# Performance work log

Hardware: AMD Instinct MI355X
Metric: run time of the kernel (lower is better)

Reference implementation:

```python
import jax, jax.numpy as jnp
import numpy as np

NEG_SLOPE = 0.2  # PyG GATConv default leaky_relu slope


def _gat_conv(x, src, dst, W, a_src, a_dst, b, num_nodes):
    # Linear transform: [N, F_out]
    h = x @ W
    # Per-node attention halves (heads=1): [N]
    alpha_s = h @ a_src
    alpha_d = h @ a_dst
    # Per-edge raw score for edge j->i: a_src.h_j + a_dst.h_i
    e = jax.nn.leaky_relu(alpha_s[src] + alpha_d[dst], NEG_SLOPE)
    # Softmax over edges grouped by destination node (numerically stable)
    m = jax.ops.segment_max(e, dst, num_segments=num_nodes)
    ex = jnp.exp(e - m[dst])
    denom = jax.ops.segment_sum(ex, dst, num_segments=num_nodes)
    coef = ex / denom[dst]
    # Attention-weighted aggregation of source features into destinations
    out = jax.ops.segment_sum(h[src] * coef[:, None], dst, num_segments=num_nodes)
    return out + b


def setup_inputs() -> dict:
    key = jax.random.key(0)
    ks = jax.random.split(key, 12)
    N, F_in, F_hid, F_out, E = 100000, 128, 64, 40, 1600000
    x = jax.random.normal(ks[0], (N, F_in), dtype=jnp.float32)
    edge_index = jax.random.randint(ks[1], (2, E), 0, N, dtype=jnp.int64)
    g = lambda k, shape, fan: jax.random.normal(k, shape, dtype=jnp.float32) * (1.0 / np.sqrt(fan))
    return {
        "x": x,
        "edge_index": edge_index,
        "W1": g(ks[2], (F_in, F_hid), F_in),
        "a_src1": g(ks[3], (F_hid,), F_hid),
        "a_dst1": g(ks[4], (F_hid,), F_hid),
        "b1": jnp.zeros((F_hid,), dtype=jnp.float32),
        "W2": g(ks[5], (F_hid, F_out), F_hid),
        "a_src2": g(ks[6], (F_out,), F_out),
        "a_dst2": g(ks[7], (F_out,), F_out),
        "b2": jnp.zeros((F_out,), dtype=jnp.float32),
    }


def reference(x, edge_index, W1, a_src1, a_dst1, b1, W2, a_src2, a_dst2, b2):
    N = x.shape[0]
    # PyG GATConv adds self loops by default
    loops = jnp.arange(N, dtype=edge_index.dtype)
    src = jnp.concatenate([edge_index[0], loops])
    dst = jnp.concatenate([edge_index[1], loops])
    h = _gat_conv(x, src, dst, W1, a_src1, a_dst1, b1, N)
    h = jax.nn.relu(h)
    # dropout p=0.5 is inactive in eval mode
    h = _gat_conv(h, src, dst, W2, a_src2, a_dst2, b2, N)
    return jax.nn.log_softmax(h, axis=-1)
```

## Files before the change

kernel.cpp:

```cpp
#include <hip/hip_runtime.h>
#include <math.h>


constexpr int F_IN = 128;
constexpr int F_H  = 64;
constexpr int F_O  = 40;
constexpr int NBMAX = 512;
constexpr int CHUNK = 8192;

__device__ __forceinline__ unsigned f2bf(float f) {
    unsigned u = __float_as_uint(f);
    return (u + 0x7FFFu + ((u >> 16) & 1u)) >> 16;
}
__device__ __forceinline__ float bflo(unsigned u) { return __uint_as_float(u << 16); }
__device__ __forceinline__ float bfhi(unsigned u) { return __uint_as_float(u & 0xFFFF0000u); }


__global__ __launch_bounds__(256) void k_binA(const int* __restrict__ dsts,
                                              int* __restrict__ bcnt,
                                              int E, int Et, int NB) {
    __shared__ int hist[NBMAX];
    for (int i = threadIdx.x; i < NB; i += 256) hist[i] = 0;
    __syncthreads();
    int e0 = blockIdx.x * 2048;
#pragma unroll
    for (int it = 0; it < 8; ++it) {
        int e = e0 + it * 256 + threadIdx.x;
        if (e < Et) {
            int d = (e < E) ? dsts[e] : (e - E);
            atomicAdd(&hist[d >> 8], 1);
        }
    }
    __syncthreads();
    for (int i = threadIdx.x; i < NB; i += 256) {
        int c = hist[i];
        if (c) atomicAdd(&bcnt[i], c);
    }
}

__global__ __launch_bounds__(NBMAX) void k_binB(const int* __restrict__ bcnt,
                                                int* __restrict__ bbase,
                                                int* __restrict__ bcur,
                                                int* __restrict__ rp,
                                                int NB, int N, int Et) {
    __shared__ int sc[NBMAX];
    int t = threadIdx.x;
    int v = (t < NB) ? bcnt[t] : 0;
    sc[t] = v; __syncthreads();
    int x = v;
    for (int o = 1; o < NBMAX; o <<= 1) {
        int y = (t >= o) ? sc[t - o] : 0;
        __syncthreads();
        x += y;
        sc[t] = x;
        __syncthreads();
    }
    if (t < NB) { int b = x - v; bbase[t] = b; bcur[t] = b; }
    if (t == 0) rp[N] = Et;
}

__global__ __launch_bounds__(256) void k_binC(const int* __restrict__ srcs,
                                              const int* __restrict__ dsts,
                                              int* __restrict__ bcur,
                                              unsigned* __restrict__ binned,
                                              int E, int Et, int NB) {
    __shared__ int hist[NBMAX];
    __shared__ int gbase[NBMAX];
    __shared__ int lcnt[NBMAX];
    int t = threadIdx.x;
    for (int i = t; i < NB; i += 256) hist[i] = 0;
    __syncthreads();
    int e0 = blockIdx.x * CHUNK;
#pragma unroll 4
    for (int it = 0; it < CHUNK / 256; ++it) {
        int e = e0 + it * 256 + t;
        if (e < Et) {
            int d = (e < E) ? dsts[e] : (e - E);
            atomicAdd(&hist[d >> 8], 1);
        }
    }
    __syncthreads();
    for (int i = t; i < NB; i += 256) {
        int c = hist[i];
        gbase[i] = c ? atomicAdd(&bcur[i], c) : 0;
        lcnt[i] = 0;
    }
    __syncthreads();
#pragma unroll 4
    for (int it = 0; it < CHUNK / 256; ++it) {
        int e = e0 + it * 256 + t;
        if (e < Et) {
            int s, d;
            if (e < E) { s = srcs[e]; d = dsts[e]; } else { s = e - E; d = s; }
            int b = d >> 8;
            int p = atomicAdd(&lcnt[b], 1);
            binned[gbase[b] + p] = (unsigned)s | ((unsigned)(d & 255) << 24);
        }
    }
}

__global__ __launch_bounds__(256) void k_binD(const unsigned* __restrict__ binned,
                                              const int* __restrict__ bbase,
                                              const int* __restrict__ bcur,
                                              int* __restrict__ rp,
                                              int* __restrict__ csr, int N) {
    __shared__ int hist[256];
    __shared__ int sc[256];
    __shared__ int lcnt[256];
    int b = blockIdx.x, t = threadIdx.x;
    int base = bbase[b], end = bcur[b];
    hist[t] = 0; __syncthreads();
    for (int j = base + t; j < end; j += 256)
        atomicAdd(&hist[binned[j] >> 24], 1);
    __syncthreads();
    int v = hist[t];
    sc[t] = v; __syncthreads();
    int x = v;
    for (int o = 1; o < 256; o <<= 1) {
        int y = (t >= o) ? sc[t - o] : 0;
        __syncthreads();
        x += y;
        sc[t] = x;
        __syncthreads();
    }
    int pref = x - v;
    int g = (b << 8) + t;
    if (g < N) rp[g] = base + pref;
    sc[t] = pref;
    lcnt[t] = 0;
    __syncthreads();
    for (int j = base + t; j < end; j += 256) {
        unsigned w = binned[j];
        int v2 = (int)(w >> 24);
        int s = (int)(w & 0xFFFFFFu);
        int p = atomicAdd(&lcnt[v2], 1);
        csr[base + sc[v2] + p] = s;
    }
}


__global__ __launch_bounds__(256) void k_gemm1(const float* __restrict__ x,
                                               const float* __restrict__ W,
                                               const float* __restrict__ avs,
                                               const float* __restrict__ avd,
                                               unsigned short* __restrict__ h,
                                               float* __restrict__ as,
                                               float* __restrict__ ad, int N) {
    __shared__ __align__(16) float Ws[F_IN * F_H];
    for (int i = threadIdx.x; i < F_IN * F_H; i += 256) Ws[i] = W[i];
    __syncthreads();
    int t = threadIdx.x;
    int r0 = blockIdx.x * 64 + (t >> 4) * 4;
    int c0 = (t & 15) * 4;
    if (r0 >= N) return;
    const float* xp = x + (size_t)r0 * F_IN;
    float acc[4][4] = {};
    for (int k4 = 0; k4 < F_IN / 4; ++k4) {
        int kb = k4 * 4;
        float4 w0 = *(const float4*)&Ws[(kb + 0) * F_H + c0];
        float4 w1 = *(const float4*)&Ws[(kb + 1) * F_H + c0];
        float4 w2 = *(const float4*)&Ws[(kb + 2) * F_H + c0];
        float4 w3 = *(const float4*)&Ws[(kb + 3) * F_H + c0];
#pragma unroll
        for (int r = 0; r < 4; ++r) {
            float4 xv = *(const float4*)&xp[(size_t)r * F_IN + kb];
            acc[r][0] += xv.x * w0.x + xv.y * w1.x + xv.z * w2.x + xv.w * w3.x;
            acc[r][1] += xv.x * w0.y + xv.y * w1.y + xv.z * w2.y + xv.w * w3.y;
            acc[r][2] += xv.x * w0.z + xv.y * w1.z + xv.z * w2.z + xv.w * w3.z;
            acc[r][3] += xv.x * w0.w + xv.y * w1.w + xv.z * w2.w + xv.w * w3.w;
        }
    }
    float4 avs4 = *(const float4*)&avs[c0];
    float4 avd4 = *(const float4*)&avd[c0];
#pragma unroll
    for (int r = 0; r < 4; ++r) {
        unsigned lo = f2bf(acc[r][0]) | (f2bf(acc[r][1]) << 16);
        unsigned hi = f2bf(acc[r][2]) | (f2bf(acc[r][3]) << 16);
        ((uint2*)h)[((size_t)(r0 + r) * F_H + c0) >> 2] = make_uint2(lo, hi);
        float ps = acc[r][0] * avs4.x + acc[r][1] * avs4.y + acc[r][2] * avs4.z + acc[r][3] * avs4.w;
        float pd = acc[r][0] * avd4.x + acc[r][1] * avd4.y + acc[r][2] * avd4.z + acc[r][3] * avd4.w;
#pragma unroll
        for (int o = 8; o; o >>= 1) {
            ps += __shfl_xor(ps, o, 16);
            pd += __shfl_xor(pd, o, 16);
        }
        if ((t & 15) == 0) { as[r0 + r] = ps; ad[r0 + r] = pd; }
    }
}


__global__ __launch_bounds__(256) void k_gemm2(const float* __restrict__ xin,
                                               const float* __restrict__ W,
                                               const float* __restrict__ avs,
                                               const float* __restrict__ avd,
                                               unsigned short* __restrict__ h,
                                               float* __restrict__ as,
                                               float* __restrict__ ad, int N) {
    __shared__ __align__(16) float Ws[F_H * F_O];
    for (int i = threadIdx.x; i < F_H * F_O; i += 256) Ws[i] = W[i];
    __syncthreads();
    int t = threadIdx.x;
    int r0 = blockIdx.x * 64 + (t >> 3) * 2;
    int l = t & 7;
    if (r0 >= N) return;
    const float4* xa = (const float4*)(xin + (size_t)r0 * F_H);
    const float4* xb = (const float4*)(xin + (size_t)(r0 + 1) * F_H);
    float acca[5] = {}, accb[5] = {};
#pragma unroll
    for (int k4 = 0; k4 < F_H / 4; ++k4) {
        float4 xva = xa[k4];
        float4 xvb = xb[k4];
        int kb = k4 * 4;
#pragma unroll
        for (int kk = 0; kk < 4; ++kk) {
            const float* wr = &Ws[(kb + kk) * F_O + l];
            float w0 = wr[0], w1 = wr[8], w2 = wr[16], w3 = wr[24], w4 = wr[32];
            float xs = (&xva.x)[kk];
            acca[0] += xs * w0; acca[1] += xs * w1; acca[2] += xs * w2;
            acca[3] += xs * w3; acca[4] += xs * w4;
            float ys = (&xvb.x)[kk];
            accb[0] += ys * w0; accb[1] += ys * w1; accb[2] += ys * w2;
            accb[3] += ys * w3; accb[4] += ys * w4;
        }
    }
    float psa = 0.f, pda = 0.f, psb = 0.f, pdb = 0.f;
    unsigned short* ra = h + (size_t)r0 * F_H;
    unsigned short* rb = h + (size_t)(r0 + 1) * F_H;
#pragma unroll
    for (int cc = 0; cc < 5; ++cc) {
        int c = l + 8 * cc;
        ra[c] = (unsigned short)f2bf(acca[cc]);
        rb[c] = (unsigned short)f2bf(accb[cc]);
        float vs = avs[c], vd = avd[c];
        psa += acca[cc] * vs; pda += acca[cc] * vd;
        psb += accb[cc] * vs; pdb += accb[cc] * vd;
    }
#pragma unroll
    for (int pp = 0; pp < 3; ++pp) {
        int c = 40 + l * 3 + pp;
        ra[c] = 0; rb[c] = 0;
    }
#pragma unroll
    for (int o = 4; o; o >>= 1) {
        psa += __shfl_xor(psa, o, 8);
        pda += __shfl_xor(pda, o, 8);
        psb += __shfl_xor(psb, o, 8);
        pdb += __shfl_xor(pdb, o, 8);
    }
    if (l == 0) { as[r0] = psa; ad[r0] = pda; as[r0 + 1] = psb; ad[r0 + 1] = pdb; }
}


template <int FOUT, bool RELU, bool LOGSM>
__global__ __launch_bounds__(256) void k_agg(const int* __restrict__ rp,
                                             const int* __restrict__ csr,
                                             const float* __restrict__ as,
                                             const float* __restrict__ ad,
                                             const uint4* __restrict__ h4,
                                             const float* __restrict__ bias,
                                             float* __restrict__ out, int N) {
    constexpr int DMAX = 256;
    __shared__ uint2 wsb[4][DMAX];
    int wslot = threadIdx.x >> 6;
    int lane = threadIdx.x & 63;
    int i = (blockIdx.x * 256 + threadIdx.x) >> 6;
    if (i >= N) return;
    int start = rp[i], end = rp[i + 1];
    int deg = end - start;
    int dm = min(deg, DMAX);
    int dmR = (dm + 31) & ~31;
    float adi = ad[i];
    float sacc = 0.f;
    for (int idx = lane; idx < dm; idx += 64) {
        int srcn = csr[start + idx];
        float e = as[srcn] + adi;
        e = (e > 0.f) ? e : 0.2f * e;
        float w = __expf(e);
        sacc += w;
        wsb[wslot][idx] = make_uint2(__float_as_uint(w), (unsigned)srcn);
    }
    {
        int idx = dm + lane;
        if (idx < dmR) wsb[wslot][idx] = make_uint2(0u, (unsigned)i);
    }

    int grp = lane >> 3, c = lane & 7;
    float acc[8] = {}, acc2[8] = {};

    for (int jb = start + dm; jb < end; jb += 8) {
        int j = jb + grp;
        bool valid = (j < end);
        int srcn = valid ? csr[j] : i;
        float e = as[srcn] + adi;
        e = (e > 0.f) ? e : 0.2f * e;
        float w = valid ? __expf(e) : 0.f;
        if (c == 0) sacc += w;
        uint4 hv = h4[(size_t)srcn * 8 + c];
        acc[0] += w * bflo(hv.x); acc[1] += w * bfhi(hv.x);
        acc[2] += w * bflo(hv.y); acc[3] += w * bfhi(hv.y);
        acc[4] += w * bflo(hv.z); acc[5] += w * bfhi(hv.z);
        acc[6] += w * bflo(hv.w); acc[7] += w * bfhi(hv.w);
    }

    for (int off = 0; off < dmR; off += 32) {
        uint2 t0 = wsb[wslot][off + grp];
        uint2 t1 = wsb[wslot][off + 8 + grp];
        uint2 t2 = wsb[wslot][off + 16 + grp];
        uint2 t3 = wsb[wslot][off + 24 + grp];
        uint4 hv0 = h4[(size_t)t0.y * 8 + c];
        uint4 hv1 = h4[(size_t)t1.y * 8 + c];
        uint4 hv2 = h4[(size_t)t2.y * 8 + c];
        uint4 hv3 = h4[(size_t)t3.y * 8 + c];
        float w0 = __uint_as_float(t0.x);
        float w1 = __uint_as_float(t1.x);
        float w2 = __uint_as_float(t2.x);
        float w3 = __uint_as_float(t3.x);
        acc[0] += w0 * bflo(hv0.x); acc[1] += w0 * bfhi(hv0.x);
        acc[2] += w0 * bflo(hv0.y); acc[3] += w0 * bfhi(hv0.y);
        acc[4] += w0 * bflo(hv0.z); acc[5] += w0 * bfhi(hv0.z);
        acc[6] += w0 * bflo(hv0.w); acc[7] += w0 * bfhi(hv0.w);
        acc2[0] += w1 * bflo(hv1.x); acc2[1] += w1 * bfhi(hv1.x);
        acc2[2] += w1 * bflo(hv1.y); acc2[3] += w1 * bfhi(hv1.y);
        acc2[4] += w1 * bflo(hv1.z); acc2[5] += w1 * bfhi(hv1.z);
        acc2[6] += w1 * bflo(hv1.w); acc2[7] += w1 * bfhi(hv1.w);
        acc[0] += w2 * bflo(hv2.x); acc[1] += w2 * bfhi(hv2.x);
        acc[2] += w2 * bflo(hv2.y); acc[3] += w2 * bfhi(hv2.y);
        acc[4] += w2 * bflo(hv2.z); acc[5] += w2 * bfhi(hv2.z);
        acc[6] += w2 * bflo(hv2.w); acc[7] += w2 * bfhi(hv2.w);
        acc2[0] += w3 * bflo(hv3.x); acc2[1] += w3 * bfhi(hv3.x);
        acc2[2] += w3 * bflo(hv3.y); acc2[3] += w3 * bfhi(hv3.y);
        acc2[4] += w3 * bflo(hv3.z); acc2[5] += w3 * bfhi(hv3.z);
        acc2[6] += w3 * bflo(hv3.w); acc2[7] += w3 * bfhi(hv3.w);
    }
#pragma unroll
    for (int k = 0; k < 8; ++k) acc[k] += acc2[k];
#pragma unroll
    for (int o = 8; o <= 32; o <<= 1)
#pragma unroll
        for (int k = 0; k < 8; ++k) acc[k] += __shfl_xor(acc[k], o);
#pragma unroll
    for (int o = 32; o; o >>= 1) sacc += __shfl_xor(sacc, o);
    float inv = 1.f / sacc;

    if (!LOGSM) {
        if (lane < 8) {
            float r[8];
#pragma unroll
            for (int k = 0; k < 8; ++k) {
                r[k] = acc[k] * inv + bias[8 * lane + k];
                if (RELU) r[k] = fmaxf(r[k], 0.f);
            }
            float4* op = (float4*)(out + (size_t)i * FOUT + 8 * lane);
            op[0] = make_float4(r[0], r[1], r[2], r[3]);
            op[1] = make_float4(r[4], r[5], r[6], r[7]);
        }
    } else {
        constexpr int VC = FOUT / 8;
        bool act = (lane < VC);
        float v[8];
#pragma unroll
        for (int k = 0; k < 8; ++k)
            v[k] = act ? (acc[k] * inv + bias[8 * lane + k]) : -INFINITY;
        float mx = v[0];
#pragma unroll
        for (int k = 1; k < 8; ++k) mx = fmaxf(mx, v[k]);
#pragma unroll
        for (int o = 1; o <= 4; o <<= 1) mx = fmaxf(mx, __shfl_xor(mx, o));
        float es = 0.f;
        if (act) {
#pragma unroll
            for (int k = 0; k < 8; ++k) es += __expf(v[k] - mx);
        }
#pragma unroll
        for (int o = 1; o <= 4; o <<= 1) es += __shfl_xor(es, o);
        if (act) {
            float lse = mx + __logf(es);
            float4* op = (float4*)(out + (size_t)i * FOUT + 8 * lane);
            op[0] = make_float4(v[0] - lse, v[1] - lse, v[2] - lse, v[3] - lse);
            op[1] = make_float4(v[4] - lse, v[5] - lse, v[6] - lse, v[7] - lse);
        }
    }
}


extern "C" void kernel_launch(void* const* d_in, const int* in_sizes, int n_in,
                              void* d_out, int out_size, void* d_ws, size_t ws_size,
                              hipStream_t stream) {
    const float* x   = (const float*)d_in[0];
    const int* edges = (const int*)d_in[1];
    const float* W1  = (const float*)d_in[2];
    const float* av_s1 = (const float*)d_in[3];
    const float* av_d1 = (const float*)d_in[4];
    const float* b1  = (const float*)d_in[5];
    const float* W2  = (const float*)d_in[6];
    const float* av_s2 = (const float*)d_in[7];
    const float* av_d2 = (const float*)d_in[8];
    const float* b2  = (const float*)d_in[9];
    float* out = (float*)d_out;

    const int N  = in_sizes[0] / F_IN;
    const int E  = in_sizes[1] / 2;
    const int Et = E + N;
    const int NB = (N + 255) >> 8;

    char* p = (char*)d_ws;
    auto alloc = [&](size_t bytes) {
        char* q = p;
        p += (bytes + 255) & ~(size_t)255;
        return (void*)q;
    };
    unsigned short* h1 = (unsigned short*)alloc((size_t)N * F_H * 2);
    float* out1   = (float*)alloc((size_t)N * F_H * 4);
    float* as1    = (float*)alloc((size_t)N * 4);
    float* ad1    = (float*)alloc((size_t)N * 4);
    float* as2    = (float*)alloc((size_t)N * 4);
    float* ad2    = (float*)alloc((size_t)N * 4);
    int* rp       = (int*)alloc((size_t)(N + 1) * 4);
    int* bcnt     = (int*)alloc(NBMAX * 4);
    int* bbase    = (int*)alloc(NBMAX * 4);
    int* bcur     = (int*)alloc(NBMAX * 4);
    unsigned* binned = (unsigned*)alloc((size_t)Et * 4);
    int* csr      = (int*)alloc((size_t)Et * 4);
    (void)n_in; (void)out_size; (void)ws_size;

    const int* srcs = edges;
    const int* dsts = edges + E;

    hipMemsetAsync(bcnt, 0, NBMAX * 4, stream);

    k_binA<<<(Et + 2047) / 2048, 256, 0, stream>>>(dsts, bcnt, E, Et, NB);
    k_binB<<<1, NBMAX, 0, stream>>>(bcnt, bbase, bcur, rp, NB, N, Et);
    k_binC<<<(Et + CHUNK - 1) / CHUNK, 256, 0, stream>>>(srcs, dsts, bcur, binned, E, Et, NB);
    k_binD<<<NB, 256, 0, stream>>>(binned, bbase, bcur, rp, csr, N);

    k_gemm1<<<(N + 63) / 64, 256, 0, stream>>>(x, W1, av_s1, av_d1, h1, as1, ad1, N);
    int gAgg = (N + 3) / 4;
    k_agg<F_H, true, false><<<gAgg, 256, 0, stream>>>(rp, csr, as1, ad1,
                                                      (const uint4*)h1, b1, out1, N);
    k_gemm2<<<(N + 63) / 64, 256, 0, stream>>>(out1, W2, av_s2, av_d2, h1, as2, ad2, N);
    k_agg<F_O, false, true><<<gAgg, 256, 0, stream>>>(rp, csr, as2, ad2,
                                                      (const uint4*)h1, b2, out, N);
}
```

Before: 333.3 us.

## Shrink CSR bins to 128 nodes and stream aggregation via wave shuffles

Node bins for the CSR construction shrink from 256 to 128 nodes, doubling the bin count. This gives k_binD twice as many blocks, and k_binB now scans four bins per thread. The aggregation kernel drops its LDS staging of weights and source indices plus the separate high-degree tail loop. It now processes 64 edges per iteration, broadcasting indices and weights with wave shuffles, and skips the second half when fewer than 32 remain. This removes LDS traffic and the two-phase structure but wastes lanes on low-degree nodes.

```diff
diff --git a/kernel.cpp b/kernel.cpp
--- a/kernel.cpp
+++ b/kernel.cpp
@@ -5,7 +5,9 @@
 constexpr int F_IN = 128;
 constexpr int F_H  = 64;
 constexpr int F_O  = 40;
-constexpr int NBMAX = 512;
+constexpr int BSH  = 7;
+constexpr int BNODES = 1 << BSH;
+constexpr int NBMAX = 1024;
 constexpr int CHUNK = 8192;
 
 __device__ __forceinline__ unsigned f2bf(float f) {
@@ -28,7 +30,7 @@
         int e = e0 + it * 256 + threadIdx.x;
         if (e < Et) {
             int d = (e < E) ? dsts[e] : (e - E);
-            atomicAdd(&hist[d >> 8], 1);
+            atomicAdd(&hist[d >> BSH], 1);
         }
     }
     __syncthreads();
@@ -38,24 +40,33 @@
     }
 }
 
-__global__ __launch_bounds__(NBMAX) void k_binB(const int* __restrict__ bcnt,
-                                                int* __restrict__ bbase,
-                                                int* __restrict__ bcur,
-                                                int* __restrict__ rp,
-                                                int NB, int N, int Et) {
-    __shared__ int sc[NBMAX];
+__global__ __launch_bounds__(256) void k_binB(const int* __restrict__ bcnt,
+                                              int* __restrict__ bbase,
+                                              int* __restrict__ bcur,
+                                              int* __restrict__ rp,
+                                              int NB, int N, int Et) {
+    __shared__ int lds[256];
     int t = threadIdx.x;
-    int v = (t < NB) ? bcnt[t] : 0;
-    sc[t] = v; __syncthreads();
-    int x = v;
-    for (int o = 1; o < NBMAX; o <<= 1) {
-        int y = (t >= o) ? sc[t - o] : 0;
+    int b4 = t * 4;
+    int v0 = (b4 + 0 < NB) ? bcnt[b4 + 0] : 0;
+    int v1 = (b4 + 1 < NB) ? bcnt[b4 + 1] : 0;
+    int v2 = (b4 + 2 < NB) ? bcnt[b4 + 2] : 0;
+    int v3 = (b4 + 3 < NB) ? bcnt[b4 + 3] : 0;
+    int tot = v0 + v1 + v2 + v3;
+    lds[t] = tot; __syncthreads();
+    int x = tot;
+    for (int o = 1; o < 256; o <<= 1) {
+        int y = (t >= o) ? lds[t - o] : 0;
         __syncthreads();
         x += y;
-        sc[t] = x;
+        lds[t] = x;
         __syncthreads();
     }
-    if (t < NB) { int b = x - v; bbase[t] = b; bcur[t] = b; }
+    int ex = x - tot;
+    if (b4 + 0 < NB) { bbase[b4 + 0] = ex; bcur[b4 + 0] = ex; } ex += v0;
+    if (b4 + 1 < NB) { bbase[b4 + 1] = ex; bcur[b4 + 1] = ex; } ex += v1;
+    if (b4 + 2 < NB) { bbase[b4 + 2] = ex; bcur[b4 + 2] = ex; } ex += v2;
+    if (b4 + 3 < NB) { bbase[b4 + 3] = ex; bcur[b4 + 3] = ex; }
     if (t == 0) rp[N] = Et;
 }
 
@@ -76,7 +87,7 @@
         int e = e0 + it * 256 + t;
         if (e < Et) {
             int d = (e < E) ? dsts[e] : (e - E);
-            atomicAdd(&hist[d >> 8], 1);
+            atomicAdd(&hist[d >> BSH], 1);
         }
     }
     __syncthreads();
@@ -92,9 +103,9 @@
         if (e < Et) {
             int s, d;
             if (e < E) { s = srcs[e]; d = dsts[e]; } else { s = e - E; d = s; }
-            int b = d >> 8;
+            int b = d >> BSH;
             int p = atomicAdd(&lcnt[b], 1);
-            binned[gbase[b] + p] = (unsigned)s | ((unsigned)(d & 255) << 24);
+            binned[gbase[b] + p] = (unsigned)s | ((unsigned)(d & (BNODES - 1)) << 24);
         }
     }
 }
@@ -104,19 +115,20 @@
                                               const int* __restrict__ bcur,
                                               int* __restrict__ rp,
                                               int* __restrict__ csr, int N) {
-    __shared__ int hist[256];
+    __shared__ int hist[BNODES];
     __shared__ int sc[256];
-    __shared__ int lcnt[256];
+    __shared__ int lcnt[BNODES];
     int b = blockIdx.x, t = threadIdx.x;
     int base = bbase[b], end = bcur[b];
-    hist[t] = 0; __syncthreads();
+    if (t < BNODES) hist[t] = 0;
+    __syncthreads();
     for (int j = base + t; j < end; j += 256)
         atomicAdd(&hist[binned[j] >> 24], 1);
     __syncthreads();
-    int v = hist[t];
+    int v = (t < BNODES) ? hist[t] : 0;
     sc[t] = v; __syncthreads();
     int x = v;
-    for (int o = 1; o < 256; o <<= 1) {
+    for (int o = 1; o < BNODES; o <<= 1) {
         int y = (t >= o) ? sc[t - o] : 0;
         __syncthreads();
         x += y;
@@ -124,10 +136,9 @@
         __syncthreads();
     }
     int pref = x - v;
-    int g = (b << 8) + t;
-    if (g < N) rp[g] = base + pref;
-    sc[t] = pref;
-    lcnt[t] = 0;
+    int g = (b << BSH) + t;
+    if (t < BNODES && g < N) rp[g] = base + pref;
+    if (t < BNODES) { sc[t] = pref; lcnt[t] = 0; }
     __syncthreads();
     for (int j = base + t; j < end; j += 256) {
         unsigned w = binned[j];
@@ -259,62 +270,35 @@
                                              const uint4* __restrict__ h4,
                                              const float* __restrict__ bias,
                                              float* __restrict__ out, int N) {
-    constexpr int DMAX = 256;
-    __shared__ uint2 wsb[4][DMAX];
-    int wslot = threadIdx.x >> 6;
     int lane = threadIdx.x & 63;
     int i = (blockIdx.x * 256 + threadIdx.x) >> 6;
     if (i >= N) return;
     int start = rp[i], end = rp[i + 1];
-    int deg = end - start;
-    int dm = min(deg, DMAX);
-    int dmR = (dm + 31) & ~31;
     float adi = ad[i];
+    int grp = lane >> 3, c = lane & 7;
+    float acc[8] = {}, acc2[8] = {};
     float sacc = 0.f;
-    for (int idx = lane; idx < dm; idx += 64) {
-        int srcn = csr[start + idx];
+
+    for (int base = start; base < end; base += 64) {
+        int cnt = end - base; if (cnt > 64) cnt = 64;
+        int srcn = i;
+        if (lane < cnt) srcn = csr[base + lane];
+        int s0 = __shfl(srcn, grp, 64);
+        int s1 = __shfl(srcn, 8 + grp, 64);
+        int s2 = __shfl(srcn, 16 + grp, 64);
+        int s3 = __shfl(srcn, 24 + grp, 64);
+        uint4 hv0 = h4[(size_t)s0 * 8 + c];
+        uint4 hv1 = h4[(size_t)s1 * 8 + c];
+        uint4 hv2 = h4[(size_t)s2 * 8 + c];
+        uint4 hv3 = h4[(size_t)s3 * 8 + c];
         float e = as[srcn] + adi;
         e = (e > 0.f) ? e : 0.2f * e;
-        float w = __expf(e);
+        float w = (lane < cnt) ? __expf(e) : 0.f;
         sacc += w;
-        wsb[wslot][idx] = make_uint2(__float_as_uint(w), (unsigned)srcn);
-    }
-    {
-        int idx = dm + lane;
-        if (idx < dmR) wsb[wslot][idx] = make_uint2(0u, (unsigned)i);
-    }
-
-    int grp = lane >> 3, c = lane & 7;
-    float acc[8] = {}, acc2[8] = {};
-
-    for (int jb = start + dm; jb < end; jb += 8) {
-        int j = jb + grp;
-        bool valid = (j < end);
-        int srcn = valid ? csr[j] : i;
-        float e = as[srcn] + adi;
-        e = (e > 0.f) ? e : 0.2f * e;
-        float w = valid ? __expf(e) : 0.f;
-        if (c == 0) sacc += w;
-        uint4 hv = h4[(size_t)srcn * 8 + c];
-        acc[0] += w * bflo(hv.x); acc[1] += w * bfhi(hv.x);
-        acc[2] += w * bflo(hv.y); acc[3] += w * bfhi(hv.y);
-        acc[4] += w * bflo(hv.z); acc[5] += w * bfhi(hv.z);
-        acc[6] += w * bflo(hv.w); acc[7] += w * bfhi(hv.w);
-    }
-
-    for (int off = 0; off < dmR; off += 32) {
-        uint2 t0 = wsb[wslot][off + grp];
-        uint2 t1 = wsb[wslot][off + 8 + grp];
-        uint2 t2 = wsb[wslot][off + 16 + grp];
-        uint2 t3 = wsb[wslot][off + 24 + grp];
-        uint4 hv0 = h4[(size_t)t0.y * 8 + c];
-        uint4 hv1 = h4[(size_t)t1.y * 8 + c];
-        uint4 hv2 = h4[(size_t)t2.y * 8 + c];
-        uint4 hv3 = h4[(size_t)t3.y * 8 + c];
-        float w0 = __uint_as_float(t0.x);
-        float w1 = __uint_as_float(t1.x);
-        float w2 = __uint_as_float(t2.x);
-        float w3 = __uint_as_float(t3.x);
+        float w0 = __shfl(w, grp, 64);
+        float w1 = __shfl(w, 8 + grp, 64);
+        float w2 = __shfl(w, 16 + grp, 64);
+        float w3 = __shfl(w, 24 + grp, 64);
         acc[0] += w0 * bflo(hv0.x); acc[1] += w0 * bfhi(hv0.x);
         acc[2] += w0 * bflo(hv0.y); acc[3] += w0 * bfhi(hv0.y);
         acc[4] += w0 * bflo(hv0.z); acc[5] += w0 * bfhi(hv0.z);
@@ -331,6 +315,37 @@
         acc2[2] += w3 * bflo(hv3.y); acc2[3] += w3 * bfhi(hv3.y);
         acc2[4] += w3 * bflo(hv3.z); acc2[5] += w3 * bfhi(hv3.z);
         acc2[6] += w3 * bflo(hv3.w); acc2[7] += w3 * bfhi(hv3.w);
+
+        if (cnt > 32) {
+            int t0 = __shfl(srcn, 32 + grp, 64);
+            int t1 = __shfl(srcn, 40 + grp, 64);
+            int t2 = __shfl(srcn, 48 + grp, 64);
+            int t3 = __shfl(srcn, 56 + grp, 64);
+            uint4 gv0 = h4[(size_t)t0 * 8 + c];
+            uint4 gv1 = h4[(size_t)t1 * 8 + c];
+            uint4 gv2 = h4[(size_t)t2 * 8 + c];
+            uint4 gv3 = h4[(size_t)t3 * 8 + c];
+            float u0 = __shfl(w, 32 + grp, 64);
+            float u1 = __shfl(w, 40 + grp, 64);
+            float u2 = __shfl(w, 48 + grp, 64);
+            float u3 = __shfl(w, 56 + grp, 64);
+            acc[0] += u0 * bflo(gv0.x); acc[1] += u0 * bfhi(gv0.x);
+            acc[2] += u0 * bflo(gv0.y); acc[3] += u0 * bfhi(gv0.y);
+            acc[4] += u0 * bflo(gv0.z); acc[5] += u0 * bfhi(gv0.z);
+            acc[6] += u0 * bflo(gv0.w); acc[7] += u0 * bfhi(gv0.w);
+            acc2[0] += u1 * bflo(gv1.x); acc2[1] += u1 * bfhi(gv1.x);
+            acc2[2] += u1 * bflo(gv1.y); acc2[3] += u1 * bfhi(gv1.y);
+            acc2[4] += u1 * bflo(gv1.z); acc2[5] += u1 * bfhi(gv1.z);
+            acc2[6] += u1 * bflo(gv1.w); acc2[7] += u1 * bfhi(gv1.w);
+            acc[0] += u2 * bflo(gv2.x); acc[1] += u2 * bfhi(gv2.x);
+            acc[2] += u2 * bflo(gv2.y); acc[3] += u2 * bfhi(gv2.y);
+            acc[4] += u2 * bflo(gv2.z); acc[5] += u2 * bfhi(gv2.z);
+            acc[6] += u2 * bflo(gv2.w); acc[7] += u2 * bfhi(gv2.w);
+            acc2[0] += u3 * bflo(gv3.x); acc2[1] += u3 * bfhi(gv3.x);
+            acc2[2] += u3 * bflo(gv3.y); acc2[3] += u3 * bfhi(gv3.y);
+            acc2[4] += u3 * bflo(gv3.z); acc2[5] += u3 * bfhi(gv3.z);
+            acc2[6] += u3 * bflo(gv3.w); acc2[7] += u3 * bfhi(gv3.w);
+        }
     }
 #pragma unroll
     for (int k = 0; k < 8; ++k) acc[k] += acc2[k];
@@ -401,7 +416,7 @@
     const int N  = in_sizes[0] / F_IN;
     const int E  = in_sizes[1] / 2;
     const int Et = E + N;
-    const int NB = (N + 255) >> 8;
+    const int NB = (N + BNODES - 1) >> BSH;
 
     char* p = (char*)d_ws;
     auto alloc = [&](size_t bytes) {
@@ -429,7 +444,7 @@
     hipMemsetAsync(bcnt, 0, NBMAX * 4, stream);
 
     k_binA<<<(Et + 2047) / 2048, 256, 0, stream>>>(dsts, bcnt, E, Et, NB);
-    k_binB<<<1, NBMAX, 0, stream>>>(bcnt, bbase, bcur, rp, NB, N, Et);
+    k_binB<<<1, 256, 0, stream>>>(bcnt, bbase, bcur, rp, NB, N, Et);
     k_binC<<<(Et + CHUNK - 1) / CHUNK, 256, 0, stream>>>(srcs, dsts, bcur, binned, E, Et, NB);
     k_binD<<<NB, 256, 0, stream>>>(binned, bbase, bcur, rp, csr, N);
 
```

Result: no change. 337.7 us (+1.3%).
